# Kernel tuning notes

Hardware: AMD Instinct MI355X
Metric: run time of the kernel (lower is better)

The kernel has to match this reference:

```python
import jax, jax.numpy as jnp
import numpy as np

B, S, D = 4, 2048, 2048   # batch, seq, hidden
E, F, K = 8, 1024, 2      # experts, expert ffn dim, top-k
SF = 1024                 # shared-expert ffn dim
EPS = 1e-6


def setup_inputs() -> dict:
    key = jax.random.key(0)
    ks = jax.random.split(key, 9)
    g = lambda k, shape, scale: (jax.random.normal(k, shape, jnp.float32) * scale)
    return {
        "x": g(ks[0], (B, S, D), 1.0),
        "rms_weight": jnp.ones((D,), jnp.float32),
        "router_w": g(ks[1], (D, E), 0.02),
        "w_gate": g(ks[2], (E, D, F), 0.02),
        "w_up": g(ks[3], (E, D, F), 0.02),
        "w_down": g(ks[4], (E, F, D), 0.02),
        "sw_gate": g(ks[5], (D, SF), 0.02),
        "sw_up": g(ks[6], (D, SF), 0.02),
        "sw_down": g(ks[7], (SF, D), 0.02),
    }


def _rmsnorm(x, w, eps=EPS):
    var = jnp.mean(x * x, axis=-1, keepdims=True)
    return x * jax.lax.rsqrt(var + eps) * w


def reference(x, rms_weight, router_w, w_gate, w_up, w_down, sw_gate, sw_up, sw_down):
    b, s, d = x.shape
    e = router_w.shape[1]
    h = _rmsnorm(x, rms_weight)
    ht = h.reshape(-1, d)                      # [T, D] tokens
    t = ht.shape[0]

    # Router: softmax over experts, top-k, renormalize selected weights
    logits = ht @ router_w                     # [T, E]
    probs = jax.nn.softmax(logits, axis=-1)
    topv, topi = jax.lax.top_k(probs, K)       # [T, K]
    topv = topv / jnp.sum(topv, axis=-1, keepdims=True)
    # dense [T, E] combine weights (zero for non-selected experts)
    w_dense = jnp.zeros((t, e), ht.dtype).at[jnp.arange(t)[:, None], topi].set(topv)

    # Expert SwiGLU MLPs (grouped GEMM expressed densely over experts)
    g = jnp.einsum('td,edf->tef', ht, w_gate)  # [T, E, F]
    u = jnp.einsum('td,edf->tef', ht, w_up)
    eo = jnp.einsum('tef,efd->ted', jax.nn.silu(g) * u, w_down)  # [T, E, D]
    moe = jnp.einsum('te,ted->td', w_dense, eo)                   # weighted combine

    # Shared expert (SwiGLU)
    sh = (jax.nn.silu(ht @ sw_gate) * (ht @ sw_up)) @ sw_down

    return (moe + sh).reshape(b, s, d)
```

## Files before the change

kernel.cpp:

```cpp
#include <hip/hip_runtime.h>
#include <stdint.h>

#define T_TOK 8192
#define DDIM  2048
#define NEXP  8
#define FDIM  1024
#define CAP   25600
#define NT_M  200
#define BK    64
#define GXT   16
#define NBLK  (GXT * NT_M)
#define CPX   (NBLK / 8)
#define NRG   1728

typedef __bf16 bf16x8 __attribute__((ext_vector_type(8)));
typedef float  f32x4  __attribute__((ext_vector_type(4)));

typedef const __attribute__((address_space(1))) uint32_t* as1_u32;
typedef __attribute__((address_space(3))) uint32_t* as3_u32;

__device__ __forceinline__ void gload16(const void* g, void* l) {
  __builtin_amdgcn_global_load_lds((as1_u32)g, (as3_u32)l, 16, 0, 0);
}
__device__ __forceinline__ float bf2f(uint16_t u) {
  union { uint32_t i; float f; } v; v.i = ((uint32_t)u) << 16; return v.f;
}
__device__ __forceinline__ uint16_t f2bf(float f) {
  union { float f; uint32_t i; } v; v.f = f;
  uint32_t i = v.i;
  i += 0x7FFFu + ((i >> 16) & 1u);
  return (uint16_t)(i >> 16);
}
__device__ __forceinline__ void mk_offs(const int* __restrict__ counts, int* o) {
  int a = 0;
  #pragma unroll
  for (int e = 0; e < NEXP; e++) { o[e] = a; a += (counts[e] + 127) & ~127; }
  o[8] = a; o[9] = a + T_TOK;
}

#define SWZ(c) ((((c) >> 2) & 15) << 3)

__global__ __launch_bounds__(256) void k_prep(
    const float* __restrict__ wg, const float* __restrict__ wu,
    const float* __restrict__ sg, const float* __restrict__ su,
    const float* __restrict__ wd, const float* __restrict__ sd,
    const float* __restrict__ x, const float* __restrict__ rmsw,
    const float* __restrict__ router_w,
    uint16_t* __restrict__ wgT, uint16_t* __restrict__ wuT,
    uint16_t* __restrict__ sgT, uint16_t* __restrict__ suT,
    uint16_t* __restrict__ wdT, uint16_t* __restrict__ sdT,
    uint16_t* __restrict__ h, int* __restrict__ topi,
    float* __restrict__ topw, int* __restrict__ counts)
{
  __shared__ uint16_t lds[128 * 256];
  int flat = blockIdx.x;
  int t = threadIdx.x;
  if (flat < NRG) {
    const float* src; uint16_t* dst;
    int Csrc, Rdst, r0, c0;
    if (flat < 1152) {
      int z = flat >> 6, rem = flat & 63;
      Csrc = FDIM; Rdst = DDIM;
      r0 = (rem >> 3) << 8;
      c0 = (rem & 7) << 7;
      if (z < 8)       { src = wg + (size_t)z * DDIM * FDIM;       dst = wgT + (size_t)z * FDIM * DDIM; }
      else if (z < 16) { src = wu + (size_t)(z - 8) * DDIM * FDIM; dst = wuT + (size_t)(z - 8) * FDIM * DDIM; }
      else if (z == 16){ src = sg; dst = sgT; }
      else             { src = su; dst = suT; }
    } else {
      int f2 = flat - 1152;
      int z = f2 >> 6, rem = f2 & 63;
      Csrc = DDIM; Rdst = FDIM;
      r0 = (rem >> 4) << 8;
      c0 = (rem & 15) << 7;
      if (z < 8) { src = wd + (size_t)z * FDIM * DDIM; dst = wdT + (size_t)z * DDIM * FDIM; }
      else       { src = sd; dst = sdT; }
    }
    int sub = t >> 5;
    int cq = (t & 31) * 4;
    #pragma unroll 4
    for (int it = 0; it < 32; it++) {
      int r = it * 8 + sub;
      float4 v = *(const float4*)(src + (size_t)(r0 + r) * Csrc + c0 + cq);
      lds[(cq + 0) * 256 + (r ^ SWZ(cq + 0))] = f2bf(v.x);
      lds[(cq + 1) * 256 + (r ^ SWZ(cq + 1))] = f2bf(v.y);
      lds[(cq + 2) * 256 + (r ^ SWZ(cq + 2))] = f2bf(v.z);
      lds[(cq + 3) * 256 + (r ^ SWZ(cq + 3))] = f2bf(v.w);
    }
    __syncthreads();
    #pragma unroll 4
    for (int it = 0; it < 16; it++) {
      int chunk = it * 256 + t;
      int cl = chunk >> 5;
      int rch = (chunk & 31) * 8;
      uint4 o = *(const uint4*)(lds + cl * 256 + (rch ^ SWZ(cl)));
      *(uint4*)(dst + (size_t)(c0 + cl) * Rdst + r0 + rch) = o;
    }
  } else {
    int wv = t >> 6, lane = t & 63;
    int tok = (flat - NRG) * 4 + wv;
    const float* xr = x + (size_t)tok * DDIM;

    float4 xv[8], wv8[8];
    #pragma unroll
    for (int j = 0; j < 8; j++) {
      xv[j]  = ((const float4*)xr)[j * 64 + lane];
      wv8[j] = ((const float4*)rmsw)[j * 64 + lane];
    }
    float ss = 0.f;
    #pragma unroll
    for (int j = 0; j < 8; j++)
      ss += xv[j].x * xv[j].x + xv[j].y * xv[j].y + xv[j].z * xv[j].z + xv[j].w * xv[j].w;
    #pragma unroll
    for (int m = 32; m >= 1; m >>= 1) ss += __shfl_xor(ss, m, 64);
    float scale = rsqrtf(ss * (1.0f / DDIM) + 1e-6f);

    float hv[8][4];
    #pragma unroll
    for (int j = 0; j < 8; j++) {
      hv[j][0] = xv[j].x * scale * wv8[j].x;
      hv[j][1] = xv[j].y * scale * wv8[j].y;
      hv[j][2] = xv[j].z * scale * wv8[j].z;
      hv[j][3] = xv[j].w * scale * wv8[j].w;
      ushort4 hw;
      hw.x = f2bf(hv[j][0]); hw.y = f2bf(hv[j][1]);
      hw.z = f2bf(hv[j][2]); hw.w = f2bf(hv[j][3]);
      ((ushort4*)(h + (size_t)tok * DDIM))[j * 64 + lane] = hw;
    }

    float lp[8] = {0, 0, 0, 0, 0, 0, 0, 0};
    #pragma unroll
    for (int j = 0; j < 8; j++) {
      #pragma unroll
      for (int c = 0; c < 4; c++) {
        int d = (j * 64 + lane) * 4 + c;
        const float* rw = router_w + (size_t)d * NEXP;
        float4 a = ((const float4*)rw)[0];
        float4 b = ((const float4*)rw)[1];
        float hj = hv[j][c];
        lp[0] += hj * a.x; lp[1] += hj * a.y; lp[2] += hj * a.z; lp[3] += hj * a.w;
        lp[4] += hj * b.x; lp[5] += hj * b.y; lp[6] += hj * b.z; lp[7] += hj * b.w;
      }
    }
    #pragma unroll
    for (int m = 32; m >= 1; m >>= 1) {
      #pragma unroll
      for (int e = 0; e < 8; e++) lp[e] += __shfl_xor(lp[e], m, 64);
    }
    if (lane == 0) {
      int i0 = 0;
      for (int e = 1; e < 8; e++) if (lp[e] > lp[i0]) i0 = e;
      int i1 = (i0 == 0) ? 1 : 0;
      for (int e = 0; e < 8; e++) if (e != i0 && lp[e] > lp[i1]) i1 = e;
      float p0 = 1.f / (1.f + expf(lp[i1] - lp[i0]));
      topi[tok * 2] = i0; topi[tok * 2 + 1] = i1;
      topw[tok * 2] = p0; topw[tok * 2 + 1] = 1.f - p0;
      atomicAdd(&counts[i0], 1);
      atomicAdd(&counts[i1], 1);
    }
  }
}

__global__ __launch_bounds__(256) void k_scatter(
    const int* __restrict__ topi, const float* __restrict__ topw,
    const int* __restrict__ counts, int* __restrict__ cursor,
    int* __restrict__ tokslot, float* __restrict__ wtrow)
{
  int offs[10];
  mk_offs(counts, offs);
  int idx = blockIdx.x * 256 + threadIdx.x;
  if (idx < T_TOK * 2) {
    int t = idx >> 1, k = idx & 1;
    int e = topi[idx];
    int slot = atomicAdd(&cursor[e], 1);
    int row = offs[e] + slot;
    tokslot[row] = t * 4 + k;
    wtrow[row] = topw[idx];
  } else {
    int t = idx - T_TOK * 2;
    int row = offs[8] + t;
    tokslot[row] = t * 4 + 2;
    wtrow[row] = 1.0f;
  }
}

#define BUFA(c) (ldsu + (size_t)(c) * 16384)
#define BUFB(c) (ldsu + 8192 + (size_t)(c) * 16384)

#define XCD_REMAP()                                                            \
  int flat_ = blockIdx.y * GXT + blockIdx.x;                                   \
  int nf_ = (flat_ & 7) * CPX + (flat_ >> 3);                                  \
  int bx = nf_ & (GXT - 1);                                                    \
  int by = nf_ / GXT;

#define STAGE8(T, C) do {                                                     \
  _Pragma("unroll") for (int i_ = 0; i_ < 4; i_++) {                          \
    int G_ = w * 256 + i_ * 64 + lane;                                        \
    gload16(aSrc[i_] + (size_t)(T) * BK, BUFA(C) + G_ * 8);                   \
    gload16(bSrc[i_] + (size_t)(T) * BK, BUFB(C) + G_ * 8);                   \
  } } while (0)

#define COMPUTE_TILE(curA, curB) do {                                         \
  _Pragma("unroll") for (int ks_ = 0; ks_ < 2; ks_++) {                       \
    int ce_ = ks_ * 32 + ((lane >> 4) << 3);                                  \
    bf16x8 av_[4], bv_[4];                                                    \
    _Pragma("unroll") for (int m_ = 0; m_ < 4; m_++) {                        \
      int rr_ = wr * 64 + m_ * 16 + (lane & 15);                              \
      av_[m_] = *(const bf16x8*)((curA) + rr_ * 64 + (ce_ ^ ((rr_ & 7) << 3))); \
    }                                                                         \
    _Pragma("unroll") for (int n_ = 0; n_ < 4; n_++) {                        \
      int rr_ = wc * 64 + n_ * 16 + (lane & 15);                              \
      bv_[n_] = *(const bf16x8*)((curB) + rr_ * 64 + (ce_ ^ ((rr_ & 7) << 3))); \
    }                                                                         \
    __builtin_amdgcn_s_setprio(1);                                            \
    _Pragma("unroll") for (int m_ = 0; m_ < 4; m_++)                          \
    _Pragma("unroll") for (int n_ = 0; n_ < 4; n_++)                          \
      acc[m_][n_] = __builtin_amdgcn_mfma_f32_16x16x32_bf16(av_[m_], bv_[n_], acc[m_][n_], 0, 0, 0); \
    __builtin_amdgcn_s_setprio(0);                                            \
  } } while (0)

__global__ __launch_bounds__(256, 2) void k_stage1(
    const uint16_t* __restrict__ h, const uint16_t* __restrict__ wgT,
    const uint16_t* __restrict__ wuT, const uint16_t* __restrict__ sgT,
    const uint16_t* __restrict__ suT, const int* __restrict__ counts,
    const int* __restrict__ tokslot, uint16_t* __restrict__ A_int)
{
  __shared__ __align__(16) uint16_t ldsu[32768];

  int offs[10];
  mk_offs(counts, offs);
  XCD_REMAP();
  int row0 = by * 128;
  int end = offs[9];
  if (row0 >= end) return;
  int e = 0;
  #pragma unroll 1
  for (; e < 9; e++) if (row0 >= offs[e] && row0 < offs[e + 1]) break;
  const uint16_t* bg = (e < NEXP) ? wgT + (size_t)e * FDIM * DDIM : sgT;
  const uint16_t* bu = (e < NEXP) ? wuT + (size_t)e * FDIM * DDIM : suT;
  int f0 = bx * 64;

  int tid = threadIdx.x, lane = tid & 63, w = tid >> 6;
  int wr = w & 1, wc = w >> 1;

  const uint16_t* aSrc[4];
  const uint16_t* bSrc[4];
  #pragma unroll
  for (int i = 0; i < 4; i++) {
    int G = w * 256 + i * 64 + lane;
    int r = G >> 3, sl = G & 7;
    int gl = sl ^ (r & 7);
    int ts = tokslot[row0 + r];
    int tok = ts < 0 ? 0 : (ts >> 2);
    aSrc[i] = h + (size_t)tok * DDIM + gl * 8;
    int b = r >> 4;
    int fc = f0 + ((b >> 1) << 4) + (r & 15);
    const uint16_t* wbase = (b & 1) ? bu : bg;
    bSrc[i] = wbase + (size_t)fc * DDIM + gl * 8;
  }

  f32x4 acc[4][4] = {};
  const int NT = DDIM / BK;

  STAGE8(0, 0);
  __syncthreads();

  #pragma unroll 1
  for (int t = 0; t < NT; ++t) {
    int cur = t & 1;
    if (t + 1 < NT) STAGE8(t + 1, cur ^ 1);
    const uint16_t* curA = BUFA(cur);
    const uint16_t* curB = BUFB(cur);
    COMPUTE_TILE(curA, curB);
    __syncthreads();
  }

  #pragma unroll
  for (int m = 0; m < 4; m++) {
    #pragma unroll
    for (int p = 0; p < 2; p++) {
      #pragma unroll
      for (int r = 0; r < 4; r++) {
        int row = row0 + wr * 64 + m * 16 + ((lane >> 4) << 2) + r;
        int col = f0 + wc * 32 + p * 16 + (lane & 15);
        float g = acc[m][2 * p][r];
        float u = acc[m][2 * p + 1][r];
        float a = (g / (1.f + expf(-g))) * u;
        A_int[(size_t)row * FDIM + col] = f2bf(a);
      }
    }
  }
}

__global__ __launch_bounds__(256, 2) void k_stage2(
    const uint16_t* __restrict__ A_int, const uint16_t* __restrict__ wdT,
    const uint16_t* __restrict__ sdT, const int* __restrict__ counts,
    const int* __restrict__ tokslot, const float* __restrict__ wtrow,
    uint16_t* __restrict__ eo, float* __restrict__ out)
{
  __shared__ __align__(16) uint16_t ldsu[32768];

  int offs[10];
  mk_offs(counts, offs);
  XCD_REMAP();
  int row0 = by * 128;
  int end = offs[9];
  if (row0 >= end) return;
  int e = 0;
  #pragma unroll 1
  for (; e < 9; e++) if (row0 >= offs[e] && row0 < offs[e + 1]) break;
  const uint16_t* bw = (e < NEXP) ? wdT + (size_t)e * DDIM * FDIM : sdT;
  int d0 = bx * 128;

  int tid = threadIdx.x, lane = tid & 63, w = tid >> 6;
  int wr = w & 1, wc = w >> 1;

  const uint16_t* aSrc[4];
  const uint16_t* bSrc[4];
  #pragma unroll
  for (int i = 0; i < 4; i++) {
    int G = w * 256 + i * 64 + lane;
    int r = G >> 3, sl = G & 7;
    int gl = sl ^ (r & 7);
    aSrc[i] = A_int + (size_t)(row0 + r) * FDIM + gl * 8;
    bSrc[i] = bw + (size_t)(d0 + r) * FDIM + gl * 8;
  }

  f32x4 acc[4][4] = {};
  const int NT = FDIM / BK;

  STAGE8(0, 0);
  __syncthreads();

  #pragma unroll 1
  for (int t = 0; t < NT; ++t) {
    int cur = t & 1;
    if (t + 1 < NT) STAGE8(t + 1, cur ^ 1);
    const uint16_t* curA = BUFA(cur);
    const uint16_t* curB = BUFB(cur);
    COMPUTE_TILE(curA, curB);
    __syncthreads();
  }

  #pragma unroll
  for (int m = 0; m < 4; m++) {
    #pragma unroll
    for (int r = 0; r < 4; r++) {
      int grow = row0 + wr * 64 + m * 16 + ((lane >> 4) << 2) + r;
      int ts = tokslot[grow];
      if (ts < 0) continue;
      int tok = ts >> 2, slot = ts & 3;
      if (slot == 2) {
        size_t obase = (size_t)tok * DDIM;
        #pragma unroll
        for (int n = 0; n < 4; n++) {
          int col = d0 + wc * 64 + n * 16 + (lane & 15);
          out[obase + col] = acc[m][n][r];
        }
      } else {
        float wt = wtrow[grow];
        size_t obase = ((size_t)tok * 2 + slot) * DDIM;
        #pragma unroll
        for (int n = 0; n < 4; n++) {
          int col = d0 + wc * 64 + n * 16 + (lane & 15);
          eo[obase + col] = f2bf(acc[m][n][r] * wt);
        }
      }
    }
  }
}

__global__ __launch_bounds__(256) void k_final(
    const uint16_t* __restrict__ eo, float* __restrict__ out)
{
  int tok = blockIdx.x;
  int col = threadIdx.x * 8;
  const uint16_t* e0 = eo + ((size_t)tok * 2) * DDIM + col;
  const uint16_t* e1 = eo + ((size_t)tok * 2 + 1) * DDIM + col;
  float* op = out + (size_t)tok * DDIM + col;
  ushort4 a0 = *(const ushort4*)(e0);
  ushort4 a1 = *(const ushort4*)(e0 + 4);
  ushort4 b0 = *(const ushort4*)(e1);
  ushort4 b1 = *(const ushort4*)(e1 + 4);
  float4 s0 = *(const float4*)(op);
  float4 s1 = *(const float4*)(op + 4);
  float4 o0, o1;
  o0.x = s0.x + bf2f(a0.x) + bf2f(b0.x);
  o0.y = s0.y + bf2f(a0.y) + bf2f(b0.y);
  o0.z = s0.z + bf2f(a0.z) + bf2f(b0.z);
  o0.w = s0.w + bf2f(a0.w) + bf2f(b0.w);
  o1.x = s1.x + bf2f(a1.x) + bf2f(b1.x);
  o1.y = s1.y + bf2f(a1.y) + bf2f(b1.y);
  o1.z = s1.z + bf2f(a1.z) + bf2f(b1.z);
  o1.w = s1.w + bf2f(a1.w) + bf2f(b1.w);
  *(float4*)(op) = o0;
  *(float4*)(op + 4) = o1;
}

extern "C" void kernel_launch(void* const* d_in, const int* in_sizes, int n_in,
                              void* d_out, int out_size, void* d_ws, size_t ws_size,
                              hipStream_t stream) {
  (void)in_sizes; (void)n_in; (void)out_size;
  const float* x    = (const float*)d_in[0];
  const float* rmsw = (const float*)d_in[1];
  const float* rtw  = (const float*)d_in[2];
  const float* wg   = (const float*)d_in[3];
  const float* wu   = (const float*)d_in[4];
  const float* wd   = (const float*)d_in[5];
  const float* sg   = (const float*)d_in[6];
  const float* su   = (const float*)d_in[7];
  const float* sd   = (const float*)d_in[8];
  float* out = (float*)d_out;

  char* base = (char*)d_ws;
  size_t off_b = 0;
  auto place = [&](size_t bytes) { size_t r = off_b; off_b += (bytes + 255) & ~(size_t)255; return r; };
  size_t o_topi    = place((size_t)T_TOK * 2 * 4);
  size_t o_topw    = place((size_t)T_TOK * 2 * 4);
  size_t o_counts  = place(64);
  size_t o_cursor  = place(64);
  size_t o_tokslot = place((size_t)CAP * 4);
  size_t o_wtrow   = place((size_t)CAP * 4);
  size_t o_h   = place((size_t)T_TOK * DDIM * 2);
  size_t o_wgT = place((size_t)NEXP * FDIM * DDIM * 2);
  size_t o_wuT = place((size_t)NEXP * FDIM * DDIM * 2);
  size_t o_sgT = place((size_t)FDIM * DDIM * 2);
  size_t o_suT = place((size_t)FDIM * DDIM * 2);
  size_t o_wdT = place((size_t)NEXP * DDIM * FDIM * 2);
  size_t o_sdT = place((size_t)DDIM * FDIM * 2);
  size_t o_Ai  = place((size_t)CAP * FDIM * 2);
  size_t o_eo  = o_h;
  size_t NEED = off_b;
  if (ws_size < NEED) return;

  int*      topi    = (int*)(base + o_topi);
  float*    topw    = (float*)(base + o_topw);
  int*      counts  = (int*)(base + o_counts);
  int*      cursor  = (int*)(base + o_cursor);
  int*      tokslot = (int*)(base + o_tokslot);
  float*    wtrow   = (float*)(base + o_wtrow);
  uint16_t* h       = (uint16_t*)(base + o_h);
  uint16_t* wgT     = (uint16_t*)(base + o_wgT);
  uint16_t* wuT     = (uint16_t*)(base + o_wuT);
  uint16_t* sgT     = (uint16_t*)(base + o_sgT);
  uint16_t* suT     = (uint16_t*)(base + o_suT);
  uint16_t* wdT     = (uint16_t*)(base + o_wdT);
  uint16_t* sdT     = (uint16_t*)(base + o_sdT);
  uint16_t* Ai      = (uint16_t*)(base + o_Ai);
  uint16_t* eo      = (uint16_t*)(base + o_eo);

  hipMemsetAsync(counts, 0, 512, stream);
  hipMemsetAsync(tokslot, 0xFF, (size_t)CAP * 4, stream);

  k_prep<<<NRG + T_TOK / 4, 256, 0, stream>>>(
      wg, wu, sg, su, wd, sd, x, rmsw, rtw,
      wgT, wuT, sgT, suT, wdT, sdT, h, topi, topw, counts);

  k_scatter<<<(T_TOK * 3) / 256, 256, 0, stream>>>(topi, topw, counts, cursor, tokslot, wtrow);

  k_stage1<<<dim3(GXT, NT_M), 256, 0, stream>>>(h, wgT, wuT, sgT, suT, counts, tokslot, Ai);
  k_stage2<<<dim3(GXT, NT_M), 256, 0, stream>>>(Ai, wdT, sdT, counts, tokslot, wtrow, eo, out);
  k_final<<<T_TOK, 256, 0, stream>>>(eo, out);
}
```

Before: 717.8 us.

## Move down-projection weight transpose from prep kernel into stage1 extra blocks

The fp32-to-bf16 transpose of the expert and shared down-projection weights moves out of the prep kernel and into extra blocks appended to the stage1 grid, which run alongside the gate/up GEMM. This shortens the prep kernel on the critical path and hides the transpose behind stage1 compute. Stage2 still reads wdT after stage1 completes, so ordering is preserved. The risk is that the memory-bound transpose blocks compete with the GEMM blocks for bandwidth and occupancy, and they may be scheduled late, since XCD remapping applies only to the GEMM blocks.

```diff
diff --git a/kernel.cpp b/kernel.cpp
--- a/kernel.cpp
+++ b/kernel.cpp
@@ -11,7 +11,8 @@
 #define GXT   16
 #define NBLK  (GXT * NT_M)
 #define CPX   (NBLK / 8)
-#define NRG   1728
+#define NRG_GU 1152
+#define NWD_Y  36
 
 typedef __bf16 bf16x8 __attribute__((ext_vector_type(8)));
 typedef float  f32x4  __attribute__((ext_vector_type(4)));
@@ -40,65 +41,58 @@
 
 #define SWZ(c) ((((c) >> 2) & 15) << 3)
 
+__device__ __forceinline__ void tr_region(
+    const float* __restrict__ src, uint16_t* __restrict__ dst,
+    int Csrc, int Rdst, int r0, int c0, uint16_t* lds, int t)
+{
+  int sub = t >> 5;
+  int cq = (t & 31) * 4;
+  #pragma unroll 4
+  for (int it = 0; it < 32; it++) {
+    int r = it * 8 + sub;
+    float4 v = *(const float4*)(src + (size_t)(r0 + r) * Csrc + c0 + cq);
+    lds[(cq + 0) * 256 + (r ^ SWZ(cq + 0))] = f2bf(v.x);
+    lds[(cq + 1) * 256 + (r ^ SWZ(cq + 1))] = f2bf(v.y);
+    lds[(cq + 2) * 256 + (r ^ SWZ(cq + 2))] = f2bf(v.z);
+    lds[(cq + 3) * 256 + (r ^ SWZ(cq + 3))] = f2bf(v.w);
+  }
+  __syncthreads();
+  #pragma unroll 4
+  for (int it = 0; it < 16; it++) {
+    int chunk = it * 256 + t;
+    int cl = chunk >> 5;
+    int rch = (chunk & 31) * 8;
+    uint4 o = *(const uint4*)(lds + cl * 256 + (rch ^ SWZ(cl)));
+    *(uint4*)(dst + (size_t)(c0 + cl) * Rdst + r0 + rch) = o;
+  }
+}
+
 __global__ __launch_bounds__(256) void k_prep(
     const float* __restrict__ wg, const float* __restrict__ wu,
     const float* __restrict__ sg, const float* __restrict__ su,
-    const float* __restrict__ wd, const float* __restrict__ sd,
     const float* __restrict__ x, const float* __restrict__ rmsw,
     const float* __restrict__ router_w,
     uint16_t* __restrict__ wgT, uint16_t* __restrict__ wuT,
     uint16_t* __restrict__ sgT, uint16_t* __restrict__ suT,
-    uint16_t* __restrict__ wdT, uint16_t* __restrict__ sdT,
     uint16_t* __restrict__ h, int* __restrict__ topi,
     float* __restrict__ topw, int* __restrict__ counts)
 {
   __shared__ uint16_t lds[128 * 256];
   int flat = blockIdx.x;
   int t = threadIdx.x;
-  if (flat < NRG) {
+  if (flat < NRG_GU) {
+    int z = flat >> 6, rem = flat & 63;
+    int r0 = (rem >> 3) << 8;
+    int c0 = (rem & 7) << 7;
     const float* src; uint16_t* dst;
-    int Csrc, Rdst, r0, c0;
-    if (flat < 1152) {
-      int z = flat >> 6, rem = flat & 63;
-      Csrc = FDIM; Rdst = DDIM;
-      r0 = (rem >> 3) << 8;
-      c0 = (rem & 7) << 7;
-      if (z < 8)       { src = wg + (size_t)z * DDIM * FDIM;       dst = wgT + (size_t)z * FDIM * DDIM; }
-      else if (z < 16) { src = wu + (size_t)(z - 8) * DDIM * FDIM; dst = wuT + (size_t)(z - 8) * FDIM * DDIM; }
-      else if (z == 16){ src = sg; dst = sgT; }
-      else             { src = su; dst = suT; }
-    } else {
-      int f2 = flat - 1152;
-      int z = f2 >> 6, rem = f2 & 63;
-      Csrc = DDIM; Rdst = FDIM;
-      r0 = (rem >> 4) << 8;
-      c0 = (rem & 15) << 7;
-      if (z < 8) { src = wd + (size_t)z * FDIM * DDIM; dst = wdT + (size_t)z * DDIM * FDIM; }
-      else       { src = sd; dst = sdT; }
-    }
-    int sub = t >> 5;
-    int cq = (t & 31) * 4;
-    #pragma unroll 4
-    for (int it = 0; it < 32; it++) {
-      int r = it * 8 + sub;
-      float4 v = *(const float4*)(src + (size_t)(r0 + r) * Csrc + c0 + cq);
-      lds[(cq + 0) * 256 + (r ^ SWZ(cq + 0))] = f2bf(v.x);
-      lds[(cq + 1) * 256 + (r ^ SWZ(cq + 1))] = f2bf(v.y);
-      lds[(cq + 2) * 256 + (r ^ SWZ(cq + 2))] = f2bf(v.z);
-      lds[(cq + 3) * 256 + (r ^ SWZ(cq + 3))] = f2bf(v.w);
-    }
-    __syncthreads();
-    #pragma unroll 4
-    for (int it = 0; it < 16; it++) {
-      int chunk = it * 256 + t;
-      int cl = chunk >> 5;
-      int rch = (chunk & 31) * 8;
-      uint4 o = *(const uint4*)(lds + cl * 256 + (rch ^ SWZ(cl)));
-      *(uint4*)(dst + (size_t)(c0 + cl) * Rdst + r0 + rch) = o;
-    }
+    if (z < 8)       { src = wg + (size_t)z * DDIM * FDIM;       dst = wgT + (size_t)z * FDIM * DDIM; }
+    else if (z < 16) { src = wu + (size_t)(z - 8) * DDIM * FDIM; dst = wuT + (size_t)(z - 8) * FDIM * DDIM; }
+    else if (z == 16){ src = sg; dst = sgT; }
+    else             { src = su; dst = suT; }
+    tr_region(src, dst, FDIM, DDIM, r0, c0, lds, t);
   } else {
     int wv = t >> 6, lane = t & 63;
-    int tok = (flat - NRG) * 4 + wv;
+    int tok = (flat - NRG_GU) * 4 + wv;
     const float* xr = x + (size_t)tok * DDIM;
 
     float4 xv[8], wv8[8];
@@ -223,9 +217,23 @@
     const uint16_t* __restrict__ h, const uint16_t* __restrict__ wgT,
     const uint16_t* __restrict__ wuT, const uint16_t* __restrict__ sgT,
     const uint16_t* __restrict__ suT, const int* __restrict__ counts,
-    const int* __restrict__ tokslot, uint16_t* __restrict__ A_int)
+    const int* __restrict__ tokslot, uint16_t* __restrict__ A_int,
+    const float* __restrict__ wd, const float* __restrict__ sd,
+    uint16_t* __restrict__ wdT, uint16_t* __restrict__ sdT)
 {
   __shared__ __align__(16) uint16_t ldsu[32768];
+
+  if (blockIdx.y >= NT_M) {
+    int f2 = (blockIdx.y - NT_M) * GXT + blockIdx.x;
+    int z = f2 >> 6, rem = f2 & 63;
+    int r0 = (rem >> 4) << 8;
+    int c0 = (rem & 15) << 7;
+    const float* src; uint16_t* dst;
+    if (z < 8) { src = wd + (size_t)z * FDIM * DDIM; dst = wdT + (size_t)z * DDIM * FDIM; }
+    else       { src = sd; dst = sdT; }
+    tr_region(src, dst, DDIM, FDIM, r0, c0, ldsu, threadIdx.x);
+    return;
+  }
 
   int offs[10];
   mk_offs(counts, offs);
@@ -452,13 +460,14 @@
   hipMemsetAsync(counts, 0, 512, stream);
   hipMemsetAsync(tokslot, 0xFF, (size_t)CAP * 4, stream);
 
-  k_prep<<<NRG + T_TOK / 4, 256, 0, stream>>>(
-      wg, wu, sg, su, wd, sd, x, rmsw, rtw,
-      wgT, wuT, sgT, suT, wdT, sdT, h, topi, topw, counts);
+  k_prep<<<NRG_GU + T_TOK / 4, 256, 0, stream>>>(
+      wg, wu, sg, su, x, rmsw, rtw,
+      wgT, wuT, sgT, suT, h, topi, topw, counts);
 
   k_scatter<<<(T_TOK * 3) / 256, 256, 0, stream>>>(topi, topw, counts, cursor, tokslot, wtrow);
 
-  k_stage1<<<dim3(GXT, NT_M), 256, 0, stream>>>(h, wgT, wuT, sgT, suT, counts, tokslot, Ai);
+  k_stage1<<<dim3(GXT, NT_M + NWD_Y), 256, 0, stream>>>(
+      h, wgT, wuT, sgT, suT, counts, tokslot, Ai, wd, sd, wdT, sdT);
   k_stage2<<<dim3(GXT, NT_M), 256, 0, stream>>>(Ai, wdT, sdT, counts, tokslot, wtrow, eo, out);
   k_final<<<T_TOK, 256, 0, stream>>>(eo, out);
 }
```

Result: slower. 733.2 us (+2.1%).
